# Optimization experiments

Hardware: AMD Instinct MI355X
Metric: run time of the kernel (lower is better)

## Reference

```python
import jax, jax.numpy as jnp
import numpy as np

B, S, D, H = 32, 8192, 128, 256  # batch-of-MLPs, seq_len, emb_dim, hidden_dim
LN_EPS = 1e-5


def setup_inputs() -> dict:
    key = jax.random.key(0)
    k0, k1, k2, k3 = jax.random.split(key, 4)
    x = jax.random.normal(k0, (B, S, D), dtype=jnp.float32)
    # shared learned Q projection (torch Linear stores W as [out,in]; y = x @ W.T)
    Wq = jax.random.normal(k1, (D, D), dtype=jnp.float32) / np.float32(np.sqrt(D))
    # per-batch-index (non-shared) fast-weight MLP params
    W1 = jax.random.normal(k2, (B, D, H), dtype=jnp.float32) / np.float32(np.sqrt(D))
    b1 = jnp.zeros((B, H), dtype=jnp.float32)
    W2 = jax.random.normal(k3, (B, H, D), dtype=jnp.float32) / np.float32(np.sqrt(H))
    b2 = jnp.zeros((B, D), dtype=jnp.float32)
    gamma = jnp.ones((B, D), dtype=jnp.float32)
    beta = jnp.zeros((B, D), dtype=jnp.float32)
    return dict(x=x, Wq=Wq, W1=W1, b1=b1, W2=W2, b2=b2, gamma=gamma, beta=beta)


def reference(x, Wq, W1, b1, W2, b2, gamma, beta):
    # queries = silu(Q(x))
    q = jax.nn.silu(jnp.einsum('bsd,ed->bse', x, Wq))
    # torch F.normalize with default dim=1 -> L2-normalize over the sequence axis
    q = q / jnp.clip(jnp.linalg.norm(q, axis=1, keepdims=True), 1e-12)
    # ParallelMLPs: per-index MLP with distinct weights (grouped GEMM), + residual
    h = jax.nn.silu(jnp.einsum('bsd,bdh->bsh', q, W1) + b1[:, None, :])
    o = jnp.einsum('bsh,bhd->bsd', h, W2) + b2[:, None, :]
    mu = jnp.mean(o, axis=-1, keepdims=True)
    var = jnp.mean(jnp.square(o - mu), axis=-1, keepdims=True)
    ln = (o - mu) / jnp.sqrt(var + LN_EPS) * gamma[:, None, :] + beta[:, None, :]
    return ln + q
```

## Files before the change

kernel.cpp:

```cpp
#include <hip/hip_runtime.h>
#include <stdint.h>

#define B_ 32
#define S_ 8192
#define D_ 128
#define H_ 256

typedef __attribute__((ext_vector_type(4))) float f32x4;
typedef __attribute__((ext_vector_type(16))) float f32x16;
typedef __attribute__((ext_vector_type(8))) short bf16x8;
typedef __attribute__((ext_vector_type(4))) unsigned int u32x4;

__device__ __forceinline__ unsigned short f2bf(float f) {
    union { float f; unsigned int u; } v; v.f = f;
    unsigned int r = v.u + 0x7fffu + ((v.u >> 16) & 1u);
    return (unsigned short)(r >> 16);
}
__device__ __forceinline__ float bf2f(unsigned short u) {
    union { unsigned int u; float f; } v; v.u = ((unsigned int)u) << 16;
    return v.f;
}
__device__ __forceinline__ float silu_f(float v) {
    return v * __builtin_amdgcn_rcpf(1.0f + __expf(-v));
}
__device__ __forceinline__ unsigned int cvtpk(float lo, float hi) {
    unsigned int r;
    asm("v_cvt_pk_bf16_f32 %0, %1, %2" : "=v"(r) : "v"(lo), "v"(hi));
    return r;
}
__device__ __forceinline__ void plswap(unsigned int& a, unsigned int& b) {
    asm("v_permlane32_swap_b32 %0, %1" : "+v"(a), "+v"(b));
}
__device__ __forceinline__ void gl16(const void* g, void* l) {
    __builtin_amdgcn_global_load_lds(
        (const __attribute__((address_space(1))) unsigned int*)g,
        (__attribute__((address_space(3))) unsigned int*)l, 16, 0, 0);
}

__global__ void k_prep(const float* __restrict__ Wq, const float* __restrict__ W1,
                       const float* __restrict__ W2, const float* __restrict__ b1,
                       unsigned short* __restrict__ wq_bf,
                       unsigned short* __restrict__ wpkg,
                       float* __restrict__ b1r) {
    __shared__ __align__(16) unsigned short tile[8192];
    int t = threadIdx.x, blk = blockIdx.x;
    if (blk < 128) {
        int b = blk >> 2, hc = blk & 3;
#pragma unroll
        for (int i = 0; i < 8; i++) {
            int idx = t + i * 256;
            int d = idx >> 4, hj = idx & 15;
            f32x4 v = *(const f32x4*)(W1 + ((size_t)(b * D_ + d)) * H_ + hc * 64 + hj * 4);
#pragma unroll
            for (int u = 0; u < 4; u++) tile[(hj * 4 + u) * 128 + d] = f2bf(v[u]);
        }
        __syncthreads();
        char* img = (char*)wpkg + (size_t)b * 131072 + (size_t)hc * 32768;
#pragma unroll
        for (int i = 0; i < 4; i++) {
            int c = t + i * 256;
            int n = c >> 9, kk = (c >> 6) & 7, l = c & 63;
            u32x4 v = *(const u32x4*)(tile + (n * 32 + (l & 31)) * 128 + kk * 16 + (l >> 5) * 8);
            *(u32x4*)(img + n * 16384 + kk * 1024 + l * 16) = v;
        }
    } else if (blk < 256) {
        int a = blk - 128;
        int b = a >> 2, hc = a & 3;
#pragma unroll
        for (int i = 0; i < 8; i++) {
            int idx = t + i * 256;
            int h = idx >> 5, d4 = idx & 31;
            f32x4 v = *(const f32x4*)(W2 + ((size_t)(b * H_ + hc * 64 + h)) * D_ + d4 * 4);
#pragma unroll
            for (int u = 0; u < 4; u++) tile[(d4 * 4 + u) * 64 + h] = f2bf(v[u]);
        }
        __syncthreads();
        char* img = (char*)wpkg + (size_t)b * 131072 + (size_t)hc * 32768;
#pragma unroll
        for (int i = 0; i < 4; i++) {
            int c = t + i * 256;
            int dn = c >> 8, n = (c >> 7) & 1, kk2 = (c >> 6) & 1, l = c & 63;
            u32x4 v = *(const u32x4*)(tile + (dn * 32 + (l & 31)) * 64 + n * 32 + kk2 * 16 + (l >> 5) * 8);
            *(u32x4*)(img + n * 16384 + 8192 + dn * 2048 + kk2 * 1024 + l * 16) = v;
        }
    } else if (blk < 320) {
        int i = (blk - 256) * 256 + t;
        wq_bf[i] = f2bf(Wq[i]);
    } else {
        int idx = (blk - 320) * 256 + t;
        int b = idx >> 8, rem = idx & 255;
        int hc = rem >> 6, n = (rem >> 5) & 1, hi = (rem >> 4) & 1, r = rem & 15;
        int h = hc * 64 + n * 32 + (r & 3) + 8 * (r >> 2) + 4 * hi;
        b1r[idx] = b1[b * H_ + h];
    }
}

__global__ __launch_bounds__(256, 2) void k_qproj(
        const float* __restrict__ x, const unsigned short* __restrict__ wq_bf,
        unsigned short* __restrict__ q_img, float* __restrict__ part) {
    __shared__ __align__(16) unsigned short lds_a[128 * 128];
    __shared__ __align__(16) unsigned short lds_b[128 * 128];
    __shared__ float lds_ss[4][128];

    int tid = threadIdx.x;
    int lane = tid & 63, w = tid >> 6;
    int g = lane >> 4, c15 = lane & 15;
    int blk = blockIdx.x;
    int b = blk >> 6, st = blk & 63;
    size_t rowbase = (size_t)b * S_ + (size_t)st * 128;
    const float* xg = x + rowbase * D_;

    char* pA = (char*)lds_a;
    char* pB = (char*)lds_b;

#pragma unroll
    for (int i = 0; i < 8; i++) {
        int idx = tid + i * 256;
        int row = idx >> 4, cb = idx & 15;
        u32x4 v = *(const u32x4*)(wq_bf + row * 128 + cb * 8);
        *(u32x4*)(pB + row * 256 + (((unsigned)cb ^ (unsigned)(row & 7)) << 4)) = v;
    }
#pragma unroll
    for (int i = 0; i < 16; i++) {
        int idx = tid + i * 256;
        int row = idx >> 5, c4 = idx & 31;
        f32x4 v = *(const f32x4*)(xg + (size_t)row * 128 + c4 * 4);
        unsigned int lo = cvtpk(v[0], v[1]), hi2 = cvtpk(v[2], v[3]);
        *(unsigned long long*)(pA + row * 256 + ((c4 * 8) ^ ((row & 7) << 4))) =
            ((unsigned long long)hi2 << 32) | (unsigned long long)lo;
    }
    __syncthreads();

    f32x4 acc[2][8];
#pragma unroll
    for (int m = 0; m < 2; m++)
#pragma unroll
        for (int n = 0; n < 8; n++) acc[m][n] = (f32x4)0.0f;

#pragma unroll
    for (int kk = 0; kk < 4; kk++) {
        int kb = kk * 64 + (g << 4);
        bf16x8 a[2];
#pragma unroll
        for (int m = 0; m < 2; m++) {
            int row = (w << 5) + (m << 4) + c15;
            a[m] = *(const bf16x8*)(pA + row * 256 + (kb ^ ((row & 7) << 4)));
        }
#pragma unroll
        for (int n = 0; n < 8; n++) {
            int rowb = (n << 4) + c15;
            bf16x8 bb = *(const bf16x8*)(pB + rowb * 256 + (kb ^ ((rowb & 7) << 4)));
#pragma unroll
            for (int m = 0; m < 2; m++)
                acc[m][n] = __builtin_amdgcn_mfma_f32_16x16x32_bf16(a[m], bb, acc[m][n], 0, 0, 0);
        }
    }

    float ss[8];
#pragma unroll
    for (int n = 0; n < 8; n++) ss[n] = 0.0f;
#pragma unroll
    for (int m = 0; m < 2; m++)
#pragma unroll
        for (int n = 0; n < 8; n++)
#pragma unroll
            for (int r = 0; r < 4; r++) {
                float v = silu_f(acc[m][n][r]);
                acc[m][n][r] = v;
                ss[n] += v * v;
            }
#pragma unroll
    for (int n = 0; n < 8; n++) {
        float v = ss[n];
        v += __shfl_xor(v, 16, 64);
        v += __shfl_xor(v, 32, 64);
        if (lane < 16) lds_ss[w][(n << 4) + lane] = v;
    }
    __syncthreads();

#pragma unroll
    for (int m = 0; m < 2; m++)
#pragma unroll
        for (int n = 0; n < 8; n++)
#pragma unroll
            for (int r = 0; r < 4; r++) {
                int row = (w << 5) + (m << 4) + (g << 2) + r;
                int col = (n << 4) + c15;
                int byte = (row >> 5) * 8192 + (col >> 4) * 1024 +
                           ((row & 31) + ((col >> 3) & 1) * 32) * 16 + (col & 7) * 2;
                *(unsigned short*)(pA + byte) = f2bf(acc[m][n][r]);
            }
    __syncthreads();

    char* qo = (char*)q_img + ((size_t)(b * 256 + st * 4)) * 8192;
#pragma unroll
    for (int i = 0; i < 8; i++) {
        int off = tid * 16 + i * 4096;
        *(u32x4*)(qo + off) = *(const u32x4*)(pA + off);
    }
    if (tid < 128) {
        float s = lds_ss[0][tid] + lds_ss[1][tid] + lds_ss[2][tid] + lds_ss[3][tid];
        part[((size_t)b * 64 + st) * 128 + tid] = s;
    }
}

__global__ void k_scale(const float* __restrict__ part, float* __restrict__ scale) {
    int idx = blockIdx.x * 256 + threadIdx.x;
    int b = idx >> 7, e = idx & 127;
    const float* p = part + (size_t)b * 64 * 128 + e;
    float s = 0.0f;
    for (int t = 0; t < 64; t++) s += p[t * 128];
    scale[idx] = 1.0f / fmaxf(sqrtf(s), 1e-12f);
}

__global__ void k_wscale(unsigned short* __restrict__ wpkg, const float* __restrict__ scale) {
    int blk = blockIdx.x;
    int b = blk >> 2;
    char* region = (char*)wpkg + (size_t)b * 131072 + (size_t)(blk & 3) * 32768;
    int t = threadIdx.x;
#pragma unroll
    for (int i = 0; i < 4; i++) {
        int c = t + i * 256;
        int n = c >> 9, kk = (c >> 6) & 7, l = c & 63;
        char* addr = region + n * 16384 + kk * 1024 + l * 16;
        int d0 = kk * 16 + (l >> 5) * 8;
        u32x4 v = *(const u32x4*)addr;
        const unsigned short* pv = (const unsigned short*)&v;
        const float* sc = scale + b * D_ + d0;
        u32x4 o;
#pragma unroll
        for (int j = 0; j < 4; j++)
            o[j] = cvtpk(bf2f(pv[2 * j]) * sc[2 * j], bf2f(pv[2 * j + 1]) * sc[2 * j + 1]);
        *(u32x4*)addr = o;
    }
}

__global__ __launch_bounds__(256, 2) void k_mlp(
        const unsigned short* __restrict__ q_img, const float* __restrict__ scale,
        const unsigned short* __restrict__ wpkg, const float* __restrict__ b1r,
        const float* __restrict__ b2, const float* __restrict__ gamma,
        const float* __restrict__ beta, float* __restrict__ out) {
    __shared__ __align__(16) char lds[33792];
    int tid = threadIdx.x;
    int lane = tid & 63, w = tid >> 6;
    int c31 = lane & 31, hi = lane >> 5;
    int blk = blockIdx.x;
    int k = blk & 7, j = blk >> 3;
    int b = k * 4 + (j >> 6);
    int st = j & 63;

    const char* wb = (const char*)wpkg + (size_t)b * 131072;
    size_t grp = (size_t)b * 256 + st * 4 + w;
    const char* qg = (const char*)q_img + grp * 8192;

    bf16x8 qf[8];
#pragma unroll
    for (int kk = 0; kk < 8; kk++)
        qf[kk] = *(const bf16x8*)(qg + kk * 1024 + lane * 16);

    gl16((const char*)b1r + (size_t)b * 1024 + lane * 16, lds + 32768);

#define STAGEPKG(p, slot) do {                                          \
    _Pragma("unroll")                                                   \
    for (int i_ = 0; i_ < 4; i_++) {                                    \
        int off_ = tid * 16 + i_ * 4096;                                \
        gl16(wb + (p) * 16384 + off_, lds + (slot) * 16384 + off_);     \
    } } while (0)

    STAGEPKG(0, 0);
    STAGEPKG(1, 1);

    f32x16 acco[4];
#pragma unroll
    for (int dn = 0; dn < 4; dn++)
#pragma unroll
        for (int e = 0; e < 16; e++) acco[dn][e] = 0.0f;

    const float* b1l = (const float*)(lds + 32768);

#pragma unroll
    for (int p = 0; p < 8; p++) {
        const int hc = p >> 1, n = p & 1, slot = p & 1;
        if (p == 7) { asm volatile("s_waitcnt vmcnt(0)" ::: "memory"); }
        else        { asm volatile("s_waitcnt vmcnt(4)" ::: "memory"); }
        __builtin_amdgcn_s_barrier();
        __builtin_amdgcn_sched_barrier(0);

        f32x16 acch;
        {
            const float* bp = b1l + (hc * 2 + n) * 32 + hi * 16;
#pragma unroll
            for (int jq = 0; jq < 4; jq++) {
                f32x4 bq = *(const f32x4*)(bp + jq * 4);
#pragma unroll
                for (int e = 0; e < 4; e++) acch[jq * 4 + e] = bq[e];
            }
        }
        const char* s0 = lds + slot * 16384;
#pragma unroll
        for (int kk = 0; kk < 8; kk++) {
            bf16x8 wf = *(const bf16x8*)(s0 + kk * 1024 + lane * 16);
            acch = __builtin_amdgcn_mfma_f32_32x32x16_bf16(wf, qf[kk], acch, 0, 0, 0);
        }
        float sv[16];
#pragma unroll
        for (int r = 0; r < 16; r++) sv[r] = silu_f(acch[r]);
        unsigned int P[8];
#pragma unroll
        for (int pp = 0; pp < 8; pp++) P[pp] = cvtpk(sv[2 * pp], sv[2 * pp + 1]);
        plswap(P[0], P[2]); plswap(P[1], P[3]);
        plswap(P[4], P[6]); plswap(P[5], P[7]);
        union { unsigned int u[4]; bf16x8 v; } f0, f1;
        f0.u[0] = P[0]; f0.u[1] = P[1]; f0.u[2] = P[2]; f0.u[3] = P[3];
        f1.u[0] = P[4]; f1.u[1] = P[5]; f1.u[2] = P[6]; f1.u[3] = P[7];
        bf16x8 pa0 = f0.v, pa1 = f1.v;
#pragma unroll
        for (int kk2 = 0; kk2 < 2; kk2++)
#pragma unroll
            for (int dn = 0; dn < 4; dn++) {
                bf16x8 wf2 = *(const bf16x8*)(s0 + 8192 + dn * 2048 + kk2 * 1024 + lane * 16);
                acco[dn] = __builtin_amdgcn_mfma_f32_32x32x16_bf16(kk2 ? pa1 : pa0, wf2,
                                                                   acco[dn], 0, 0, 0);
            }

        asm volatile("s_waitcnt lgkmcnt(0)" ::: "memory");
        __builtin_amdgcn_sched_barrier(0);
        __builtin_amdgcn_s_barrier();
        if (p < 6) STAGEPKG(p + 2, slot);
    }
#undef STAGEPKG

    __syncthreads();
    char* myq = (char*)lds + w * 8192;
#pragma unroll
    for (int kk = 0; kk < 8; kk++)
        *(bf16x8*)(myq + c31 * 256 + ((kk * 32 + hi * 16) ^ ((c31 & 7) << 4))) = qf[kk];

    float scv[4], gv[4], bev[4], b2v[4];
#pragma unroll
    for (int dn = 0; dn < 4; dn++) {
        int d = dn * 32 + c31;
        scv[dn] = scale[b * 128 + d];
        gv[dn]  = gamma[b * 128 + d];
        bev[dn] = beta[b * 128 + d];
        b2v[dn] = b2[b * 128 + d];
    }

    float* og = out + grp * 32 * 128;
#pragma unroll
    for (int r = 0; r < 16; r++) {
        float v0 = acco[0][r] + b2v[0], v1 = acco[1][r] + b2v[1];
        float v2 = acco[2][r] + b2v[2], v3 = acco[3][r] + b2v[3];
        float s1 = (v0 + v1) + (v2 + v3);
        float s2 = (v0 * v0 + v1 * v1) + (v2 * v2 + v3 * v3);
        s1 += __shfl_xor(s1, 1, 64);   s2 += __shfl_xor(s2, 1, 64);
        s1 += __shfl_xor(s1, 2, 64);   s2 += __shfl_xor(s2, 2, 64);
        s1 += __shfl_xor(s1, 4, 64);   s2 += __shfl_xor(s2, 4, 64);
        s1 += __shfl_xor(s1, 8, 64);   s2 += __shfl_xor(s2, 8, 64);
        s1 += __shfl_xor(s1, 16, 64);  s2 += __shfl_xor(s2, 16, 64);
        float mu = s1 * (1.0f / 128.0f);
        float var = s2 * (1.0f / 128.0f) - mu * mu;
        float rstd = rsqrtf(var + 1e-5f);
        int srow0 = (r & 3) + 8 * (r >> 2);
        int row = srow0 + 4 * hi;
        float vv[4] = {v0, v1, v2, v3};
#pragma unroll
        for (int dn = 0; dn < 4; dn++) {
            float qv = bf2f(*(const unsigned short*)(myq + row * 256 +
                        ((dn * 64 + c31 * 2) ^ ((row & 7) << 4)))) * scv[dn];
            float o = (vv[dn] - mu) * rstd * gv[dn] + bev[dn] + qv;
            og[(size_t)row * 128 + dn * 32 + c31] = o;
        }
    }
}

extern "C" void kernel_launch(void* const* d_in, const int* in_sizes, int n_in,
                              void* d_out, int out_size, void* d_ws, size_t ws_size,
                              hipStream_t stream) {
    (void)in_sizes; (void)n_in; (void)out_size; (void)ws_size;
    const float* x     = (const float*)d_in[0];
    const float* Wq    = (const float*)d_in[1];
    const float* W1    = (const float*)d_in[2];
    const float* b1    = (const float*)d_in[3];
    const float* W2    = (const float*)d_in[4];
    const float* b2    = (const float*)d_in[5];
    const float* gamma = (const float*)d_in[6];
    const float* beta  = (const float*)d_in[7];
    float* out = (float*)d_out;

    char* ws = (char*)d_ws;
    unsigned short* wq_bf = (unsigned short*)(ws);
    unsigned short* wpkg  = (unsigned short*)(ws + 32768);
    float* part           = (float*)(ws + 4227072);
    float* scale          = (float*)(ws + 5275648);
    float* b1r            = (float*)(ws + 5292032);
    unsigned short* q_img = (unsigned short*)(ws + 5324800);

    hipLaunchKernelGGL(k_prep, dim3(352), dim3(256), 0, stream, Wq, W1, W2, b1, wq_bf, wpkg, b1r);
    hipLaunchKernelGGL(k_qproj, dim3(2048), dim3(256), 0, stream, x, wq_bf, q_img, part);
    hipLaunchKernelGGL(k_scale, dim3(16), dim3(256), 0, stream, part, scale);
    hipLaunchKernelGGL(k_wscale, dim3(128), dim3(256), 0, stream, wpkg, scale);
    hipLaunchKernelGGL(k_mlp, dim3(2048), dim3(256), 0, stream,
                       q_img, scale, wpkg, b1r, b2, gamma, beta, out);
}
```

Before: 132.7 us.

## Load W2 directly to registers and triple-buffer W1 in LDS with one barrier

W2 fragments are no longer staged through LDS. Each wave now loads them straight from global memory into registers at the start of each step, and only W1 halves go through LDS in a three-slot ring. This removes the second barrier per step, and the next W1 prefetch is issued right after the single barrier. The first GEMM is split into two independent accumulators to shorten the MFMA dependency chain, and s_setprio is raised around the MFMA blocks. In exchange it costs more VGPRs for the W2 registers, adds redundant global/L2 reads of W2 across waves, and depends on hand-tuned vmcnt counts being correct.

```diff
diff --git a/kernel.cpp b/kernel.cpp
--- a/kernel.cpp
+++ b/kernel.cpp
@@ -260,15 +260,15 @@
 
     gl16((const char*)b1r + (size_t)b * 1024 + lane * 16, lds + 32768);
 
-#define STAGEPKG(p, slot) do {                                          \
+#define STAGEW1(p, slot) do {                                           \
     _Pragma("unroll")                                                   \
-    for (int i_ = 0; i_ < 4; i_++) {                                    \
+    for (int i_ = 0; i_ < 2; i_++) {                                    \
         int off_ = tid * 16 + i_ * 4096;                                \
-        gl16(wb + (p) * 16384 + off_, lds + (slot) * 16384 + off_);     \
+        gl16(wb + (p) * 16384 + off_, lds + (slot) * 8192 + off_);      \
     } } while (0)
 
-    STAGEPKG(0, 0);
-    STAGEPKG(1, 1);
+    STAGEW1(0, 0);
+    STAGEW1(1, 1);
 
     f32x16 acco[4];
 #pragma unroll
@@ -280,31 +280,47 @@
 
 #pragma unroll
     for (int p = 0; p < 8; p++) {
-        const int hc = p >> 1, n = p & 1, slot = p & 1;
-        if (p == 7) { asm volatile("s_waitcnt vmcnt(0)" ::: "memory"); }
-        else        { asm volatile("s_waitcnt vmcnt(4)" ::: "memory"); }
+        const int hc = p >> 1, n = p & 1, slot = p % 3;
+
+        const char* w2h = wb + p * 16384 + 8192;
+        bf16x8 w2r[8];
+#pragma unroll
+        for (int f = 0; f < 8; f++)
+            w2r[f] = *(const bf16x8*)(w2h + f * 1024 + lane * 16);
+
+        if (p < 7) asm volatile("s_waitcnt vmcnt(10)" ::: "memory");
+        else       asm volatile("s_waitcnt vmcnt(8)" ::: "memory");
         __builtin_amdgcn_s_barrier();
         __builtin_amdgcn_sched_barrier(0);
-
-        f32x16 acch;
+        if (p < 6) STAGEW1(p + 2, (p + 2) % 3);
+
+        f32x16 acch0, acch1;
         {
             const float* bp = b1l + (hc * 2 + n) * 32 + hi * 16;
 #pragma unroll
             for (int jq = 0; jq < 4; jq++) {
                 f32x4 bq = *(const f32x4*)(bp + jq * 4);
 #pragma unroll
-                for (int e = 0; e < 4; e++) acch[jq * 4 + e] = bq[e];
+                for (int e = 0; e < 4; e++) {
+                    acch0[jq * 4 + e] = bq[e];
+                    acch1[jq * 4 + e] = 0.0f;
+                }
             }
         }
-        const char* s0 = lds + slot * 16384;
-#pragma unroll
-        for (int kk = 0; kk < 8; kk++) {
-            bf16x8 wf = *(const bf16x8*)(s0 + kk * 1024 + lane * 16);
-            acch = __builtin_amdgcn_mfma_f32_32x32x16_bf16(wf, qf[kk], acch, 0, 0, 0);
-        }
+        const char* s0 = lds + slot * 8192;
+        __builtin_amdgcn_s_setprio(1);
+#pragma unroll
+        for (int kk = 0; kk < 8; kk += 2) {
+            bf16x8 wf0 = *(const bf16x8*)(s0 + kk * 1024 + lane * 16);
+            bf16x8 wf1 = *(const bf16x8*)(s0 + (kk + 1) * 1024 + lane * 16);
+            acch0 = __builtin_amdgcn_mfma_f32_32x32x16_bf16(wf0, qf[kk], acch0, 0, 0, 0);
+            acch1 = __builtin_amdgcn_mfma_f32_32x32x16_bf16(wf1, qf[kk + 1], acch1, 0, 0, 0);
+        }
+        __builtin_amdgcn_s_setprio(0);
+
         float sv[16];
 #pragma unroll
-        for (int r = 0; r < 16; r++) sv[r] = silu_f(acch[r]);
+        for (int r = 0; r < 16; r++) sv[r] = silu_f(acch0[r] + acch1[r]);
         unsigned int P[8];
 #pragma unroll
         for (int pp = 0; pp < 8; pp++) P[pp] = cvtpk(sv[2 * pp], sv[2 * pp + 1]);
@@ -314,21 +330,17 @@
         f0.u[0] = P[0]; f0.u[1] = P[1]; f0.u[2] = P[2]; f0.u[3] = P[3];
         f1.u[0] = P[4]; f1.u[1] = P[5]; f1.u[2] = P[6]; f1.u[3] = P[7];
         bf16x8 pa0 = f0.v, pa1 = f1.v;
+
+        __builtin_amdgcn_s_setprio(1);
 #pragma unroll
         for (int kk2 = 0; kk2 < 2; kk2++)
 #pragma unroll
-            for (int dn = 0; dn < 4; dn++) {
-                bf16x8 wf2 = *(const bf16x8*)(s0 + 8192 + dn * 2048 + kk2 * 1024 + lane * 16);
-                acco[dn] = __builtin_amdgcn_mfma_f32_32x32x16_bf16(kk2 ? pa1 : pa0, wf2,
-                                                                   acco[dn], 0, 0, 0);
-            }
-
-        asm volatile("s_waitcnt lgkmcnt(0)" ::: "memory");
-        __builtin_amdgcn_sched_barrier(0);
-        __builtin_amdgcn_s_barrier();
-        if (p < 6) STAGEPKG(p + 2, slot);
-    }
-#undef STAGEPKG
+            for (int dn = 0; dn < 4; dn++)
+                acco[dn] = __builtin_amdgcn_mfma_f32_32x32x16_bf16(
+                    kk2 ? pa1 : pa0, w2r[dn * 2 + kk2], acco[dn], 0, 0, 0);
+        __builtin_amdgcn_s_setprio(0);
+    }
+#undef STAGEW1
 
     __syncthreads();
     char* myq = (char*)lds + w * 8192;
```

Measured after the change: 143.5 us. +8.2%, slower.

## Process two row groups per wave in k_mlp to reuse staged weights

Applied to the files above, without the earlier changes.

Each wave in k_mlp now handles two 32-row groups instead of one. Every weight fragment read from LDS feeds two MFMAs, which halves the grid and the total weight staging traffic per output row. MFMA sections are also wrapped in s_setprio to favour matrix issue. This doubles the accumulator and q-fragment register footprint, which risks spills or lower occupancy under launch_bounds(256,2), and leaves fewer blocks to hide latency.

```diff
diff --git a/kernel.cpp b/kernel.cpp
--- a/kernel.cpp
+++ b/kernel.cpp
@@ -246,17 +246,20 @@
     int c31 = lane & 31, hi = lane >> 5;
     int blk = blockIdx.x;
     int k = blk & 7, j = blk >> 3;
-    int b = k * 4 + (j >> 6);
-    int st = j & 63;
+    int b = k * 4 + (j >> 5);
+    int st2 = j & 31;
 
     const char* wb = (const char*)wpkg + (size_t)b * 131072;
-    size_t grp = (size_t)b * 256 + st * 4 + w;
-    const char* qg = (const char*)q_img + grp * 8192;
-
-    bf16x8 qf[8];
-#pragma unroll
-    for (int kk = 0; kk < 8; kk++)
-        qf[kk] = *(const bf16x8*)(qg + kk * 1024 + lane * 16);
+    size_t g0 = (size_t)b * 256 + st2 * 8 + w * 2;
+    const char* qgA = (const char*)q_img + g0 * 8192;
+    const char* qgB = qgA + 8192;
+
+    bf16x8 qfA[8], qfB[8];
+#pragma unroll
+    for (int kk = 0; kk < 8; kk++) {
+        qfA[kk] = *(const bf16x8*)(qgA + kk * 1024 + lane * 16);
+        qfB[kk] = *(const bf16x8*)(qgB + kk * 1024 + lane * 16);
+    }
 
     gl16((const char*)b1r + (size_t)b * 1024 + lane * 16, lds + 32768);
 
@@ -270,11 +273,11 @@
     STAGEPKG(0, 0);
     STAGEPKG(1, 1);
 
-    f32x16 acco[4];
+    f32x16 accoA[4], accoB[4];
 #pragma unroll
     for (int dn = 0; dn < 4; dn++)
 #pragma unroll
-        for (int e = 0; e < 16; e++) acco[dn][e] = 0.0f;
+        for (int e = 0; e < 16; e++) { accoA[dn][e] = 0.0f; accoB[dn][e] = 0.0f; }
 
     const float* b1l = (const float*)(lds + 32768);
 
@@ -286,42 +289,70 @@
         __builtin_amdgcn_s_barrier();
         __builtin_amdgcn_sched_barrier(0);
 
-        f32x16 acch;
+        f32x16 acchA, acchB;
         {
             const float* bp = b1l + (hc * 2 + n) * 32 + hi * 16;
 #pragma unroll
             for (int jq = 0; jq < 4; jq++) {
                 f32x4 bq = *(const f32x4*)(bp + jq * 4);
 #pragma unroll
-                for (int e = 0; e < 4; e++) acch[jq * 4 + e] = bq[e];
+                for (int e = 0; e < 4; e++) {
+                    acchA[jq * 4 + e] = bq[e];
+                    acchB[jq * 4 + e] = bq[e];
+                }
             }
         }
         const char* s0 = lds + slot * 16384;
+        __builtin_amdgcn_s_setprio(1);
 #pragma unroll
         for (int kk = 0; kk < 8; kk++) {
             bf16x8 wf = *(const bf16x8*)(s0 + kk * 1024 + lane * 16);
-            acch = __builtin_amdgcn_mfma_f32_32x32x16_bf16(wf, qf[kk], acch, 0, 0, 0);
-        }
-        float sv[16];
-#pragma unroll
-        for (int r = 0; r < 16; r++) sv[r] = silu_f(acch[r]);
-        unsigned int P[8];
-#pragma unroll
-        for (int pp = 0; pp < 8; pp++) P[pp] = cvtpk(sv[2 * pp], sv[2 * pp + 1]);
-        plswap(P[0], P[2]); plswap(P[1], P[3]);
-        plswap(P[4], P[6]); plswap(P[5], P[7]);
-        union { unsigned int u[4]; bf16x8 v; } f0, f1;
-        f0.u[0] = P[0]; f0.u[1] = P[1]; f0.u[2] = P[2]; f0.u[3] = P[3];
-        f1.u[0] = P[4]; f1.u[1] = P[5]; f1.u[2] = P[6]; f1.u[3] = P[7];
-        bf16x8 pa0 = f0.v, pa1 = f1.v;
+            acchA = __builtin_amdgcn_mfma_f32_32x32x16_bf16(wf, qfA[kk], acchA, 0, 0, 0);
+            acchB = __builtin_amdgcn_mfma_f32_32x32x16_bf16(wf, qfB[kk], acchB, 0, 0, 0);
+        }
+        __builtin_amdgcn_s_setprio(0);
+        bf16x8 paA0, paA1, paB0, paB1;
+        {
+            float sv[16];
+#pragma unroll
+            for (int r = 0; r < 16; r++) sv[r] = silu_f(acchA[r]);
+            unsigned int P[8];
+#pragma unroll
+            for (int pp = 0; pp < 8; pp++) P[pp] = cvtpk(sv[2 * pp], sv[2 * pp + 1]);
+            plswap(P[0], P[2]); plswap(P[1], P[3]);
+            plswap(P[4], P[6]); plswap(P[5], P[7]);
+            union { unsigned int u[4]; bf16x8 v; } f0, f1;
+            f0.u[0] = P[0]; f0.u[1] = P[1]; f0.u[2] = P[2]; f0.u[3] = P[3];
+            f1.u[0] = P[4]; f1.u[1] = P[5]; f1.u[2] = P[6]; f1.u[3] = P[7];
+            paA0 = f0.v; paA1 = f1.v;
+        }
+        {
+            float sv[16];
+#pragma unroll
+            for (int r = 0; r < 16; r++) sv[r] = silu_f(acchB[r]);
+            unsigned int P[8];
+#pragma unroll
+            for (int pp = 0; pp < 8; pp++) P[pp] = cvtpk(sv[2 * pp], sv[2 * pp + 1]);
+            plswap(P[0], P[2]); plswap(P[1], P[3]);
+            plswap(P[4], P[6]); plswap(P[5], P[7]);
+            union { unsigned int u[4]; bf16x8 v; } f0, f1;
+            f0.u[0] = P[0]; f0.u[1] = P[1]; f0.u[2] = P[2]; f0.u[3] = P[3];
+            f1.u[0] = P[4]; f1.u[1] = P[5]; f1.u[2] = P[6]; f1.u[3] = P[7];
+            paB0 = f0.v; paB1 = f1.v;
+        }
+
+        __builtin_amdgcn_s_setprio(1);
 #pragma unroll
         for (int kk2 = 0; kk2 < 2; kk2++)
 #pragma unroll
             for (int dn = 0; dn < 4; dn++) {
                 bf16x8 wf2 = *(const bf16x8*)(s0 + 8192 + dn * 2048 + kk2 * 1024 + lane * 16);
-                acco[dn] = __builtin_amdgcn_mfma_f32_32x32x16_bf16(kk2 ? pa1 : pa0, wf2,
-                                                                   acco[dn], 0, 0, 0);
+                accoA[dn] = __builtin_amdgcn_mfma_f32_32x32x16_bf16(kk2 ? paA1 : paA0, wf2,
+                                                                    accoA[dn], 0, 0, 0);
+                accoB[dn] = __builtin_amdgcn_mfma_f32_32x32x16_bf16(kk2 ? paB1 : paB0, wf2,
+                                                                    accoB[dn], 0, 0, 0);
             }
+        __builtin_amdgcn_s_setprio(0);
 
         asm volatile("s_waitcnt lgkmcnt(0)" ::: "memory");
         __builtin_amdgcn_sched_barrier(0);
@@ -332,9 +363,6 @@
 
     __syncthreads();
     char* myq = (char*)lds + w * 8192;
-#pragma unroll
-    for (int kk = 0; kk < 8; kk++)
-        *(bf16x8*)(myq + c31 * 256 + ((kk * 32 + hi * 16) ^ ((c31 & 7) << 4))) = qf[kk];
 
     float scv[4], gv[4], bev[4], b2v[4];
 #pragma unroll
@@ -346,32 +374,40 @@
         b2v[dn] = b2[b * 128 + d];
     }
 
-    float* og = out + grp * 32 * 128;
-#pragma unroll
-    for (int r = 0; r < 16; r++) {
-        float v0 = acco[0][r] + b2v[0], v1 = acco[1][r] + b2v[1];
-        float v2 = acco[2][r] + b2v[2], v3 = acco[3][r] + b2v[3];
-        float s1 = (v0 + v1) + (v2 + v3);
-        float s2 = (v0 * v0 + v1 * v1) + (v2 * v2 + v3 * v3);
-        s1 += __shfl_xor(s1, 1, 64);   s2 += __shfl_xor(s2, 1, 64);
-        s1 += __shfl_xor(s1, 2, 64);   s2 += __shfl_xor(s2, 2, 64);
-        s1 += __shfl_xor(s1, 4, 64);   s2 += __shfl_xor(s2, 4, 64);
-        s1 += __shfl_xor(s1, 8, 64);   s2 += __shfl_xor(s2, 8, 64);
-        s1 += __shfl_xor(s1, 16, 64);  s2 += __shfl_xor(s2, 16, 64);
-        float mu = s1 * (1.0f / 128.0f);
-        float var = s2 * (1.0f / 128.0f) - mu * mu;
-        float rstd = rsqrtf(var + 1e-5f);
-        int srow0 = (r & 3) + 8 * (r >> 2);
-        int row = srow0 + 4 * hi;
-        float vv[4] = {v0, v1, v2, v3};
-#pragma unroll
-        for (int dn = 0; dn < 4; dn++) {
-            float qv = bf2f(*(const unsigned short*)(myq + row * 256 +
-                        ((dn * 64 + c31 * 2) ^ ((row & 7) << 4)))) * scv[dn];
-            float o = (vv[dn] - mu) * rstd * gv[dn] + bev[dn] + qv;
-            og[(size_t)row * 128 + dn * 32 + c31] = o;
-        }
-    }
+#define EPILOG(QF, ACCO, GRP) do {                                              \
+    _Pragma("unroll")                                                           \
+    for (int kk = 0; kk < 8; kk++)                                              \
+        *(bf16x8*)(myq + c31 * 256 + ((kk * 32 + hi * 16) ^ ((c31 & 7) << 4))) = QF[kk]; \
+    float* og = out + (GRP) * 32 * 128;                                         \
+    _Pragma("unroll")                                                           \
+    for (int r = 0; r < 16; r++) {                                              \
+        float v0 = ACCO[0][r] + b2v[0], v1 = ACCO[1][r] + b2v[1];               \
+        float v2 = ACCO[2][r] + b2v[2], v3 = ACCO[3][r] + b2v[3];               \
+        float s1 = (v0 + v1) + (v2 + v3);                                       \
+        float s2 = (v0 * v0 + v1 * v1) + (v2 * v2 + v3 * v3);                   \
+        s1 += __shfl_xor(s1, 1, 64);   s2 += __shfl_xor(s2, 1, 64);             \
+        s1 += __shfl_xor(s1, 2, 64);   s2 += __shfl_xor(s2, 2, 64);             \
+        s1 += __shfl_xor(s1, 4, 64);   s2 += __shfl_xor(s2, 4, 64);             \
+        s1 += __shfl_xor(s1, 8, 64);   s2 += __shfl_xor(s2, 8, 64);             \
+        s1 += __shfl_xor(s1, 16, 64);  s2 += __shfl_xor(s2, 16, 64);            \
+        float mu = s1 * (1.0f / 128.0f);                                        \
+        float var = s2 * (1.0f / 128.0f) - mu * mu;                             \
+        float rstd = rsqrtf(var + 1e-5f);                                       \
+        int srow0 = (r & 3) + 8 * (r >> 2);                                     \
+        int row = srow0 + 4 * hi;                                               \
+        float vv[4] = {v0, v1, v2, v3};                                         \
+        _Pragma("unroll")                                                       \
+        for (int dn = 0; dn < 4; dn++) {                                        \
+            float qv = bf2f(*(const unsigned short*)(myq + row * 256 +          \
+                        ((dn * 64 + c31 * 2) ^ ((row & 7) << 4)))) * scv[dn];   \
+            float o = (vv[dn] - mu) * rstd * gv[dn] + bev[dn] + qv;             \
+            og[(size_t)row * 128 + dn * 32 + c31] = o;                          \
+        }                                                                       \
+    } } while (0)
+
+    EPILOG(qfA, accoA, g0);
+    EPILOG(qfB, accoB, (g0 + 1));
+#undef EPILOG
 }
 
 extern "C" void kernel_launch(void* const* d_in, const int* in_sizes, int n_in,
@@ -400,6 +436,6 @@
     hipLaunchKernelGGL(k_qproj, dim3(2048), dim3(256), 0, stream, x, wq_bf, q_img, part);
     hipLaunchKernelGGL(k_scale, dim3(16), dim3(256), 0, stream, part, scale);
     hipLaunchKernelGGL(k_wscale, dim3(128), dim3(256), 0, stream, wpkg, scale);
-    hipLaunchKernelGGL(k_mlp, dim3(2048), dim3(256), 0, stream,
+    hipLaunchKernelGGL(k_mlp, dim3(1024), dim3(256), 0, stream,
                        q_img, scale, wpkg, b1r, b2, gamma, beta, out);
 }
```

Result: slower. 208.2 us (+56.9%).

## Fuse scale into weight-scaling kernel and double MLP stage width per iteration

Applied to the files above, without the earlier changes.

Merges the norm-scale reduction kernel into the weight-scaling kernel, removing one launch; each of the four blocks per batch recomputes the scale redundantly. In the MLP kernel each pipeline step now stages two hidden chunks (32KB) at once with four iterations instead of eight. Two independent MFMA accumulator chains are interleaved and s_setprio is raised around the MFMA sections. LDS doubles to 66KB and launch bounds drop to one block per SM-min, which may reduce occupancy.

```diff
diff --git a/kernel.cpp b/kernel.cpp
--- a/kernel.cpp
+++ b/kernel.cpp
@@ -204,20 +204,23 @@
     }
 }
 
-__global__ void k_scale(const float* __restrict__ part, float* __restrict__ scale) {
-    int idx = blockIdx.x * 256 + threadIdx.x;
-    int b = idx >> 7, e = idx & 127;
-    const float* p = part + (size_t)b * 64 * 128 + e;
-    float s = 0.0f;
-    for (int t = 0; t < 64; t++) s += p[t * 128];
-    scale[idx] = 1.0f / fmaxf(sqrtf(s), 1e-12f);
-}
-
-__global__ void k_wscale(unsigned short* __restrict__ wpkg, const float* __restrict__ scale) {
+__global__ void k_scalew(const float* __restrict__ part, unsigned short* __restrict__ wpkg,
+                         float* __restrict__ scale) {
+    __shared__ float sc_l[128];
     int blk = blockIdx.x;
     int b = blk >> 2;
+    int t = threadIdx.x;
+    if (t < 128) {
+        const float* p = part + (size_t)b * 8192 + t;
+        float s = 0.0f;
+#pragma unroll 8
+        for (int i = 0; i < 64; i++) s += p[i * 128];
+        float sc = 1.0f / fmaxf(sqrtf(s), 1e-12f);
+        sc_l[t] = sc;
+        if ((blk & 3) == 0) scale[b * 128 + t] = sc;
+    }
+    __syncthreads();
     char* region = (char*)wpkg + (size_t)b * 131072 + (size_t)(blk & 3) * 32768;
-    int t = threadIdx.x;
 #pragma unroll
     for (int i = 0; i < 4; i++) {
         int c = t + i * 256;
@@ -226,21 +229,21 @@
         int d0 = kk * 16 + (l >> 5) * 8;
         u32x4 v = *(const u32x4*)addr;
         const unsigned short* pv = (const unsigned short*)&v;
-        const float* sc = scale + b * D_ + d0;
         u32x4 o;
 #pragma unroll
         for (int j = 0; j < 4; j++)
-            o[j] = cvtpk(bf2f(pv[2 * j]) * sc[2 * j], bf2f(pv[2 * j + 1]) * sc[2 * j + 1]);
+            o[j] = cvtpk(bf2f(pv[2 * j]) * sc_l[d0 + 2 * j],
+                         bf2f(pv[2 * j + 1]) * sc_l[d0 + 2 * j + 1]);
         *(u32x4*)addr = o;
     }
 }
 
-__global__ __launch_bounds__(256, 2) void k_mlp(
+__global__ __launch_bounds__(256, 1) void k_mlp(
         const unsigned short* __restrict__ q_img, const float* __restrict__ scale,
         const unsigned short* __restrict__ wpkg, const float* __restrict__ b1r,
         const float* __restrict__ b2, const float* __restrict__ gamma,
         const float* __restrict__ beta, float* __restrict__ out) {
-    __shared__ __align__(16) char lds[33792];
+    __shared__ __align__(16) char lds[66560];
     int tid = threadIdx.x;
     int lane = tid & 63, w = tid >> 6;
     int c31 = lane & 31, hi = lane >> 5;
@@ -258,17 +261,17 @@
     for (int kk = 0; kk < 8; kk++)
         qf[kk] = *(const bf16x8*)(qg + kk * 1024 + lane * 16);
 
-    gl16((const char*)b1r + (size_t)b * 1024 + lane * 16, lds + 32768);
-
-#define STAGEPKG(p, slot) do {                                          \
+    gl16((const char*)b1r + (size_t)b * 1024 + lane * 16, lds + 65536);
+
+#define STAGE32(hcn, slot) do {                                         \
     _Pragma("unroll")                                                   \
-    for (int i_ = 0; i_ < 4; i_++) {                                    \
+    for (int i_ = 0; i_ < 8; i_++) {                                    \
         int off_ = tid * 16 + i_ * 4096;                                \
-        gl16(wb + (p) * 16384 + off_, lds + (slot) * 16384 + off_);     \
+        gl16(wb + (hcn) * 32768 + off_, lds + (slot) * 32768 + off_);   \
     } } while (0)
 
-    STAGEPKG(0, 0);
-    STAGEPKG(1, 1);
+    STAGE32(0, 0);
+    STAGE32(1, 1);
 
     f32x16 acco[4];
 #pragma unroll
@@ -276,59 +279,94 @@
 #pragma unroll
         for (int e = 0; e < 16; e++) acco[dn][e] = 0.0f;
 
-    const float* b1l = (const float*)(lds + 32768);
-
-#pragma unroll
-    for (int p = 0; p < 8; p++) {
-        const int hc = p >> 1, n = p & 1, slot = p & 1;
-        if (p == 7) { asm volatile("s_waitcnt vmcnt(0)" ::: "memory"); }
-        else        { asm volatile("s_waitcnt vmcnt(4)" ::: "memory"); }
+    const float* b1l = (const float*)(lds + 65536);
+
+#pragma unroll
+    for (int p = 0; p < 4; p++) {
+        const int slot = p & 1;
+        if (p == 3) { asm volatile("s_waitcnt vmcnt(0)" ::: "memory"); }
+        else        { asm volatile("s_waitcnt vmcnt(8)" ::: "memory"); }
         __builtin_amdgcn_s_barrier();
         __builtin_amdgcn_sched_barrier(0);
 
-        f32x16 acch;
+        f32x16 acch0, acch1;
         {
-            const float* bp = b1l + (hc * 2 + n) * 32 + hi * 16;
+            const float* bp0 = b1l + (p * 2 + 0) * 32 + hi * 16;
+            const float* bp1 = b1l + (p * 2 + 1) * 32 + hi * 16;
 #pragma unroll
             for (int jq = 0; jq < 4; jq++) {
-                f32x4 bq = *(const f32x4*)(bp + jq * 4);
-#pragma unroll
-                for (int e = 0; e < 4; e++) acch[jq * 4 + e] = bq[e];
+                f32x4 q0 = *(const f32x4*)(bp0 + jq * 4);
+                f32x4 q1 = *(const f32x4*)(bp1 + jq * 4);
+#pragma unroll
+                for (int e = 0; e < 4; e++) {
+                    acch0[jq * 4 + e] = q0[e];
+                    acch1[jq * 4 + e] = q1[e];
+                }
             }
         }
-        const char* s0 = lds + slot * 16384;
+        const char* s0 = lds + slot * 32768;
+        const char* s1 = s0 + 16384;
+
+        __builtin_amdgcn_s_setprio(1);
 #pragma unroll
         for (int kk = 0; kk < 8; kk++) {
-            bf16x8 wf = *(const bf16x8*)(s0 + kk * 1024 + lane * 16);
-            acch = __builtin_amdgcn_mfma_f32_32x32x16_bf16(wf, qf[kk], acch, 0, 0, 0);
-        }
-        float sv[16];
-#pragma unroll
-        for (int r = 0; r < 16; r++) sv[r] = silu_f(acch[r]);
-        unsigned int P[8];
-#pragma unroll
-        for (int pp = 0; pp < 8; pp++) P[pp] = cvtpk(sv[2 * pp], sv[2 * pp + 1]);
-        plswap(P[0], P[2]); plswap(P[1], P[3]);
-        plswap(P[4], P[6]); plswap(P[5], P[7]);
-        union { unsigned int u[4]; bf16x8 v; } f0, f1;
-        f0.u[0] = P[0]; f0.u[1] = P[1]; f0.u[2] = P[2]; f0.u[3] = P[3];
-        f1.u[0] = P[4]; f1.u[1] = P[5]; f1.u[2] = P[6]; f1.u[3] = P[7];
-        bf16x8 pa0 = f0.v, pa1 = f1.v;
+            bf16x8 wf0 = *(const bf16x8*)(s0 + kk * 1024 + lane * 16);
+            bf16x8 wf1 = *(const bf16x8*)(s1 + kk * 1024 + lane * 16);
+            acch0 = __builtin_amdgcn_mfma_f32_32x32x16_bf16(wf0, qf[kk], acch0, 0, 0, 0);
+            acch1 = __builtin_amdgcn_mfma_f32_32x32x16_bf16(wf1, qf[kk], acch1, 0, 0, 0);
+        }
+        __builtin_amdgcn_s_setprio(0);
+
+        bf16x8 pa00, pa01, pa10, pa11;
+        {
+            float sv[16];
+#pragma unroll
+            for (int r = 0; r < 16; r++) sv[r] = silu_f(acch0[r]);
+            unsigned int P[8];
+#pragma unroll
+            for (int pp = 0; pp < 8; pp++) P[pp] = cvtpk(sv[2 * pp], sv[2 * pp + 1]);
+            plswap(P[0], P[2]); plswap(P[1], P[3]);
+            plswap(P[4], P[6]); plswap(P[5], P[7]);
+            union { unsigned int u[4]; bf16x8 v; } f0, f1;
+            f0.u[0] = P[0]; f0.u[1] = P[1]; f0.u[2] = P[2]; f0.u[3] = P[3];
+            f1.u[0] = P[4]; f1.u[1] = P[5]; f1.u[2] = P[6]; f1.u[3] = P[7];
+            pa00 = f0.v; pa01 = f1.v;
+        }
+        {
+            float sv[16];
+#pragma unroll
+            for (int r = 0; r < 16; r++) sv[r] = silu_f(acch1[r]);
+            unsigned int P[8];
+#pragma unroll
+            for (int pp = 0; pp < 8; pp++) P[pp] = cvtpk(sv[2 * pp], sv[2 * pp + 1]);
+            plswap(P[0], P[2]); plswap(P[1], P[3]);
+            plswap(P[4], P[6]); plswap(P[5], P[7]);
+            union { unsigned int u[4]; bf16x8 v; } f0, f1;
+            f0.u[0] = P[0]; f0.u[1] = P[1]; f0.u[2] = P[2]; f0.u[3] = P[3];
+            f1.u[0] = P[4]; f1.u[1] = P[5]; f1.u[2] = P[6]; f1.u[3] = P[7];
+            pa10 = f0.v; pa11 = f1.v;
+        }
+
+        __builtin_amdgcn_s_setprio(1);
 #pragma unroll
         for (int kk2 = 0; kk2 < 2; kk2++)
 #pragma unroll
             for (int dn = 0; dn < 4; dn++) {
-                bf16x8 wf2 = *(const bf16x8*)(s0 + 8192 + dn * 2048 + kk2 * 1024 + lane * 16);
-                acco[dn] = __builtin_amdgcn_mfma_f32_32x32x16_bf16(kk2 ? pa1 : pa0, wf2,
+                bf16x8 wf20 = *(const bf16x8*)(s0 + 8192 + dn * 2048 + kk2 * 1024 + lane * 16);
+                bf16x8 wf21 = *(const bf16x8*)(s1 + 8192 + dn * 2048 + kk2 * 1024 + lane * 16);
+                acco[dn] = __builtin_amdgcn_mfma_f32_32x32x16_bf16(kk2 ? pa01 : pa00, wf20,
+                                                                   acco[dn], 0, 0, 0);
+                acco[dn] = __builtin_amdgcn_mfma_f32_32x32x16_bf16(kk2 ? pa11 : pa10, wf21,
                                                                    acco[dn], 0, 0, 0);
             }
+        __builtin_amdgcn_s_setprio(0);
 
         asm volatile("s_waitcnt lgkmcnt(0)" ::: "memory");
         __builtin_amdgcn_sched_barrier(0);
         __builtin_amdgcn_s_barrier();
-        if (p < 6) STAGEPKG(p + 2, slot);
-    }
-#undef STAGEPKG
+        if (p < 2) STAGE32(p + 2, slot);
+    }
+#undef STAGE32
 
     __syncthreads();
     char* myq = (char*)lds + w * 8192;
@@ -398,8 +436,7 @@
 
     hipLaunchKernelGGL(k_prep, dim3(352), dim3(256), 0, stream, Wq, W1, W2, b1, wq_bf, wpkg, b1r);
     hipLaunchKernelGGL(k_qproj, dim3(2048), dim3(256), 0, stream, x, wq_bf, q_img, part);
-    hipLaunchKernelGGL(k_scale, dim3(16), dim3(256), 0, stream, part, scale);
-    hipLaunchKernelGGL(k_wscale, dim3(128), dim3(256), 0, stream, wpkg, scale);
+    hipLaunchKernelGGL(k_scalew, dim3(128), dim3(256), 0, stream, part, wpkg, scale);
     hipLaunchKernelGGL(k_mlp, dim3(2048), dim3(256), 0, stream,
                        q_img, scale, wpkg, b1r, b2, gamma, beta, out);
 }
```

New measurement: 140.4 us. 5.8% more time.
